# Kernel optimization log

Measured on AMD Instinct MI355X. Metric: run time of the kernel, lower is better.

The kernel has to match this reference:

```python
import jax, jax.numpy as jnp
import numpy as np

EPS = 1e-8
NUM_HEADS = 8
SCALE = 25.0
SIM_THRESH = 0.75
BLOCK = 10  # per-frame proposal group size used by the zeroing mask


def _l2norm(x):
    return x / (jnp.linalg.norm(x, axis=-1, keepdims=True) + EPS)


def setup_inputs() -> dict:
    key = jax.random.key(0)
    ks = jax.random.split(key, 7)
    B, N, C = 1, 2000, 256
    H = NUM_HEADS
    x_cls = jax.random.normal(ks[0], (B, N, C), dtype=jnp.float32)
    x_reg = jax.random.normal(ks[1], (B, N, C), dtype=jnp.float32)
    cls_score = jax.random.uniform(ks[2], (N,), dtype=jnp.float32)
    fg_score = jax.random.uniform(ks[3], (N,), dtype=jnp.float32)
    coord_attn = jax.random.uniform(ks[4], (B, H, N, N), dtype=jnp.float32)
    W_qkv_cls = jax.random.normal(ks[5], (3 * C, C), dtype=jnp.float32) * 0.02
    W_qkv_reg = jax.random.normal(ks[6], (3 * C, C), dtype=jnp.float32) * 0.02
    return {"x_cls": x_cls, "x_reg": x_reg, "cls_score": cls_score,
            "fg_score": fg_score, "coord_attn": coord_attn,
            "W_qkv_cls": W_qkv_cls, "W_qkv_reg": W_qkv_reg}


def reference(x_cls, x_reg, cls_score, fg_score, coord_attn, W_qkv_cls, W_qkv_reg):
    B, N, C = x_cls.shape
    H = NUM_HEADS
    D = C // H

    def qkv(x, W):
        t = (x @ W.T).reshape(B, N, 3, H, D).transpose(2, 0, 3, 1, 4)  # [3,B,H,N,D]
        return t[0], t[1], t[2]

    q_cls, k_cls, v_cls = qkv(x_cls, W_qkv_cls)
    q_reg, k_reg, v_reg = qkv(x_reg, W_qkv_reg)

    q_cls, k_cls = _l2norm(q_cls), _l2norm(k_cls)
    q_reg, k_reg = _l2norm(q_reg), _l2norm(k_reg)
    v_cls_normed = _l2norm(v_cls)

    cs = cls_score.reshape(1, 1, 1, N)  # broadcast over [B,H,N,N]
    fs = fg_score.reshape(1, 1, 1, N)

    attn_cls_raw = jnp.einsum('bhnd,bhmd->bhnm', v_cls_normed, v_cls_normed)

    attn_cls = jax.nn.softmax(jnp.einsum('bhnd,bhmd->bhnm', q_cls, k_cls) * SCALE * cs, axis=-1)
    attn_reg = jax.nn.softmax(jnp.einsum('bhnd,bhmd->bhnm', q_reg, k_reg) * SCALE * fs, axis=-1)

    attn = (attn_reg + attn_cls) * 0.5 * coord_attn
    attn = jax.lax.stop_gradient(attn)  # original detaches before masking

    # block-diagonal zeroing: row j zeros cols [j//10*10, j//10*10+9), keep diagonal
    rows = jnp.arange(N)[:, None]
    cols = jnp.arange(N)[None, :]
    block_start = (rows // BLOCK) * BLOCK
    zero_mask = (cols >= block_start) & (cols < block_start + (BLOCK - 1)) & (cols != rows)
    attn = jnp.where(zero_mask, 0.0, attn)

    x = jnp.einsum('bhnm,bhmd->bhnd', attn, v_cls).transpose(0, 2, 1, 3).reshape(B, N, C)
    x_ori = v_cls.transpose(0, 2, 1, 3).reshape(B, N, C)
    x_cat = jnp.concatenate([x, x_ori], axis=-1)  # [B,N,2C]

    # ave=True branch
    sim_raw = jnp.sum(attn_cls_raw, axis=1)[0] / H          # [N,N]
    sim_mask = (sim_raw > SIM_THRESH).astype(x_cls.dtype)
    sim_attn = jnp.sum(attn, axis=1)[0] / H                 # [N,N]
    sim_round2 = jax.nn.softmax(sim_attn, axis=-1)
    sim_round2 = sim_mask * sim_round2 / (jnp.sum(sim_mask * sim_round2, axis=-1, keepdims=True) + EPS)
    return x_cat, sim_round2
```

## Files before the change

kernel.cpp:

```cpp
#include <hip/hip_runtime.h>
#include <math.h>

typedef _Float16 half8 __attribute__((ext_vector_type(8)));
typedef _Float16 half4 __attribute__((ext_vector_type(4)));
typedef _Float16 half2v __attribute__((ext_vector_type(2)));
typedef float f32x4 __attribute__((ext_vector_type(4)));

constexpr int N = 2000;
constexpr int NP = 2048;
constexpr int H = 8;
constexpr int D = 32;
constexpr float SCL = 25.0f;
constexpr float L2E = 1.4426950408889634f;
constexpr float FM2 = 25.0f * L2E;

#define MFMA16(a,b,c)  __builtin_amdgcn_mfma_f32_16x16x32_f16((a),(b),(c),0,0,0)
#define MFMA16K(a,b,c) __builtin_amdgcn_mfma_f32_16x16x16f16((a),(b),(c),0,0,0)

__device__ __forceinline__ float fexp2(float x) { return __builtin_amdgcn_exp2f(x); }


__global__ __launch_bounds__(256) void wconv_kernel(
    const float* __restrict__ Wc, const float* __restrict__ Wr,
    _Float16* __restrict__ Wch, _Float16* __restrict__ Wrh)
{
    const int i = blockIdx.x * 256 + threadIdx.x;
    Wch[i] = (_Float16)Wc[i];
    Wrh[i] = (_Float16)Wr[i];
}

__global__ __launch_bounds__(256) void qkv_kernel(
    const float* __restrict__ xc, const float* __restrict__ xr,
    const _Float16* __restrict__ Wch, const _Float16* __restrict__ Wrh,
    const float* __restrict__ clsScore, const float* __restrict__ fgScore,
    _Float16* __restrict__ Qch, _Float16* __restrict__ Kch,
    _Float16* __restrict__ Qrh, _Float16* __restrict__ Krh,
    _Float16* __restrict__ Vnh, _Float16* __restrict__ Vth,
    float* __restrict__ out)
{
    constexpr int XS = 264;
    __shared__ _Float16 xs[16 * XS];
    const int t = threadIdx.x;
    const int n0 = blockIdx.x * 16;
    const int by = blockIdx.y;
    const int which = (by < 3) ? by : (by - 3);
    const bool isCls = by < 3;
    const float* x = isCls ? xc : xr;
    const _Float16* Wh = isCls ? Wch : Wrh;

    #pragma unroll
    for (int it = 0; it < 4; ++it) {
        const int f = t + it * 256;
        const int row = f >> 6, c4 = f & 63;
        const float4 v = *(const float4*)(x + (size_t)(n0 + row) * 256 + c4 * 4);
        half4 hv; hv[0]=(_Float16)v.x; hv[1]=(_Float16)v.y; hv[2]=(_Float16)v.z; hv[3]=(_Float16)v.w;
        *(half4*)&xs[row * XS + c4 * 4] = hv;
    }
    __syncthreads();

    const int w = t >> 6, l = t & 63;
    const int lr = l & 15, lg = l >> 4;
    const int obase = which * 256 + w * 64;
    f32x4 acc[4] = {{0,0,0,0},{0,0,0,0},{0,0,0,0},{0,0,0,0}};
    for (int k0 = 0; k0 < 256; k0 += 32) {
        const half8 aX = *(const half8*)&xs[lr * XS + k0 + lg * 8];
        #pragma unroll
        for (int s = 0; s < 4; ++s) {
            const half8 bW = *(const half8*)(Wh + (size_t)(obase + s * 16 + lr) * 256 + k0 + lg * 8);
            acc[s] = MFMA16(aX, bW, acc[s]);
        }
    }
    f32x4 kscale = {1.f,1.f,1.f,1.f};
    if (which == 1) {
        const float* sp = isCls ? clsScore : fgScore;
        kscale = (SCL * L2E) * *(const f32x4*)(sp + n0 + lg*4);
    }
    #pragma unroll
    for (int p = 0; p < 2; ++p) {
        const int h = 2 * w + p;
        float ss[4];
        #pragma unroll
        for (int j = 0; j < 4; ++j) {
            float v = acc[2*p][j]*acc[2*p][j] + acc[2*p+1][j]*acc[2*p+1][j];
            #pragma unroll
            for (int off = 1; off < 16; off <<= 1) v += __shfl_xor(v, off);
            ss[j] = sqrtf(v) + 1e-8f;
        }
        if (which < 2) {
            _Float16* Qd = isCls ? (which == 0 ? Qch : Kch) : (which == 0 ? Qrh : Krh);
            #pragma unroll
            for (int sh = 0; sh < 2; ++sh)
                #pragma unroll
                for (int j = 0; j < 4; ++j)
                    Qd[((size_t)h*NP + n0 + lg*4 + j)*D + sh*16 + lr]
                        = (_Float16)(acc[2*p+sh][j] / ss[j] * kscale[j]);
        } else {
            #pragma unroll
            for (int sh = 0; sh < 2; ++sh) {
                const int d = sh * 16 + lr;
                half4 tv;
                #pragma unroll
                for (int j = 0; j < 4; ++j) {
                    const float raw = acc[2*p+sh][j];
                    Vnh[((size_t)h*NP + n0 + lg*4 + j)*D + d] = (_Float16)(raw / ss[j]);
                    out[(size_t)(n0 + lg*4 + j)*512 + 256 + h*D + d] = raw;
                    tv[j] = (_Float16)raw;
                }
                *(half4*)(Vth + ((size_t)h*D + d)*NP + n0 + lg*4) = tv;
            }
        }
    }
}

__global__ __launch_bounds__(512) void stats_kernel(
    const _Float16* __restrict__ Qch, const _Float16* __restrict__ Kch,
    const _Float16* __restrict__ Qrh, const _Float16* __restrict__ Krh,
    float* __restrict__ BIAS)
{
    __shared__ float Ssh[2][4][16];
    const int t = threadIdx.x;
    const int w = t >> 6, l = t & 63;
    const int nsub = w >> 2, mq = w & 3;
    const int n0 = blockIdx.x * 32 + nsub * 16;
    const int h = blockIdx.y, z = blockIdx.z;
    const _Float16* Q = z ? Qrh : Qch;
    const _Float16* K = z ? Krh : Kch;
    const int lr = l & 15, lg = l >> 4;
    const half8 aQ = *(const half8*)(Q + ((size_t)h*NP + n0 + lr)*D + lg*8);
    float S[4] = {0.f, 0.f, 0.f, 0.f};
    const int mqB0 = (mq == 0) ? 0 : 31*mq;
    const int mqB1 = (mq == 3) ? 125 : 31*(mq+1);
    half8 bK = *(const half8*)(K + ((size_t)h*NP + mqB0*16 + lr)*D + lg*8);
    for (int ms = mqB0; ms < mqB1; ++ms) {
        const half8 cur = bK;
        if (ms + 1 < mqB1)
            bK = *(const half8*)(K + ((size_t)h*NP + (ms+1)*16 + lr)*D + lg*8);
        f32x4 z4 = {0.f, 0.f, 0.f, 0.f};
        const f32x4 c = MFMA16(aQ, cur, z4);
        #pragma unroll
        for (int j = 0; j < 4; ++j) S[j] += fexp2(c[j] - FM2);
    }
    #pragma unroll
    for (int j = 0; j < 4; ++j) {
        #pragma unroll
        for (int off = 1; off < 16; off <<= 1) S[j] += __shfl_xor(S[j], off);
    }
    if (lr == 0) {
        #pragma unroll
        for (int j = 0; j < 4; ++j) Ssh[nsub][mq][lg*4 + j] = S[j];
    }
    __syncthreads();
    if (t < 32) {
        const int ns = t >> 4, rl = t & 15;
        const int n = blockIdx.x * 32 + ns*16 + rl;
        BIAS[((size_t)z*H + h)*NP + n]
            = -__log2f(Ssh[ns][0][rl] + Ssh[ns][1][rl] + Ssh[ns][2][rl] + Ssh[ns][3][rl]) - FM2 - 1.0f;
    }
}

__global__ __launch_bounds__(256) void vvmask_kernel(
    const _Float16* __restrict__ Vnh, unsigned char* __restrict__ Mask)
{
    const int t = threadIdx.x;
    const int w = t >> 6, l = t & 63;
    const int n0 = blockIdx.y * 16;
    const int m00 = blockIdx.x * 256 + w * 64;
    const int lr = l & 15, lg = l >> 4;
    half8 aV[8];
    #pragma unroll
    for (int h = 0; h < 8; ++h)
        aV[h] = *(const half8*)(Vnh + ((size_t)(h*NP + n0 + lr))*D + lg*8);
    for (int s = 0; s < 4; ++s) {
        const int mb = m00 + s*16;
        f32x4 acc = {0.f, 0.f, 0.f, 0.f};
        #pragma unroll
        for (int h = 0; h < 8; ++h) {
            const half8 bV = *(const half8*)(Vnh + ((size_t)(h*NP + mb + lr))*D + lg*8);
            acc = MFMA16(aV[h], bV, acc);
        }
        const int m = mb + lr;
        if (m < N) {
            #pragma unroll
            for (int j = 0; j < 4; ++j) {
                const int n = n0 + lg*4 + j;
                Mask[(size_t)n*N + m] = (acc[j]*0.125f > 0.75f) ? (unsigned char)1 : (unsigned char)0;
            }
        }
    }
}

__global__ __launch_bounds__(256) void attn_kernel(
    const _Float16* __restrict__ Kch, const _Float16* __restrict__ Krh,
    const _Float16* __restrict__ Qch, const _Float16* __restrict__ Qrh,
    const _Float16* __restrict__ Vth, const float* __restrict__ coord,
    const float* __restrict__ BIAS,
    _Float16* __restrict__ SIMH, _Float16* __restrict__ XPH)
{
    __shared__ __align__(16) float costage[2][2048];
    __shared__ _Float16 pvred[2][4][2][16][18];

    const int t = threadIdx.x;
    const int w = t >> 6, l = t & 63;
    const int lr = l & 15, lg = l >> 4;
    const int mc = blockIdx.x;
    const int m0 = mc * 128;
    const int n0 = blockIdx.y * 16;
    const int n  = n0 + lr;
    const int bs = (n / 10) * 10;
    const int s0 = w * 2;

    unsigned kill = 0u;
    #pragma unroll
    for (int sl = 0; sl < 2; ++sl)
        #pragma unroll
        for (int j = 0; j < 4; ++j) {
            const int m = m0 + (s0 + sl)*16 + lg*4 + j;
            if ((m >= bs && m < bs + 9 && m != n) || m >= N) kill |= (1u << (sl*4 + j));
        }

    const int drow = w*4 + (l >> 4);
    const int dck  = l & 15;
    auto DMACO = [&](int hp) {
        float* dst = &costage[hp & 1][0];
        #pragma unroll
        for (int i = 0; i < 2; ++i) {
            const int colb = i*64 + ((((dck*16) ^ ((drow & 7) << 4))) >> 2);
            unsigned gi = (unsigned)((hp*N + (n0 + drow))*N + m0 + colb);
            gi = gi < 31999996u ? gi : 31999996u;
            __builtin_amdgcn_global_load_lds(
                (const __attribute__((address_space(1))) void*)(coord + gi),
                (__attribute__((address_space(3))) void*)(dst + i*1024 + w*256),
                16, 0, 0);
        }
    };

    half8 aQc[2], aQr[2]; float bC[2], bR[2];
    auto LOADQ = [&](int hp) {
        const int hb = hp & 1;
        aQc[hb] = *(const half8*)(Qch + ((size_t)hp*NP + n)*D + lg*8);
        aQr[hb] = *(const half8*)(Qrh + ((size_t)hp*NP + n)*D + lg*8);
        bC[hb]  = BIAS[(size_t)hp*NP + n];
        bR[hb]  = BIAS[(size_t)(H + hp)*NP + n];
    };

    half8 kc[2], kr[2]; half4 v0[2], v1[2];
    auto LOADKV = [&](int hp, int sl, int b) {
        const int m = m0 + (s0 + sl)*16;
        const size_t kb = ((size_t)hp*NP + m + lr)*D + lg*8;
        kc[b] = *(const half8*)(Kch + kb);
        kr[b] = *(const half8*)(Krh + kb);
        v0[b] = *(const half4*)(Vth + ((size_t)(hp*D + lr))*NP + m + lg*4);
        v1[b] = *(const half4*)(Vth + ((size_t)(hp*D + 16 + lr))*NP + m + lg*4);
    };

    float sacc[2][4] = {{0,0,0,0},{0,0,0,0}};

    DMACO(0); LOADQ(0);
    __builtin_amdgcn_sched_barrier(0);
    LOADKV(0, 0, 0);
    asm volatile("s_waitcnt vmcnt(4)" ::: "memory");
    __builtin_amdgcn_s_barrier();
    __builtin_amdgcn_sched_barrier(0);

    #pragma unroll
    for (int h = 0; h < H; ++h) {
        const int hb = h & 1;
        if (h + 1 < H) { DMACO(h + 1); LOADQ(h + 1); }
        __builtin_amdgcn_sched_barrier(0);
        f32x4 pv0 = {0,0,0,0}, pv1 = {0,0,0,0};
        #pragma unroll
        for (int sl = 0; sl < 2; ++sl) {
            const int b = (h*2 + sl) & 1;
            if (sl == 0)            LOADKV(h, 1, b ^ 1);
            else if (h + 1 < H)     LOADKV(h + 1, 0, b ^ 1);
            const int s = s0 + sl;
            const int cbyte = (((s & 3)*64 + lg*16) ^ ((lr & 7) << 4));
            const f32x4 co = *(const f32x4*)(&costage[hb][(s >> 2)*1024 + lr*64] + (cbyte >> 2));
            f32x4 z4 = {0,0,0,0};
            const f32x4 cc = MFMA16(kc[b], aQc[hb], z4);
            const f32x4 cr = MFMA16(kr[b], aQr[hb], z4);
            half4 af;
            #pragma unroll
            for (int j = 0; j < 4; ++j) {
                float a = (fexp2(cc[j] + bC[hb]) + fexp2(cr[j] + bR[hb])) * co[j];
                if ((kill >> (sl*4 + j)) & 1u) a = 0.f;
                sacc[sl][j] += a;
                af[j] = (_Float16)a;
            }
            pv0 = MFMA16K(af, v0[b], pv0);
            pv1 = MFMA16K(af, v1[b], pv1);
        }
        {
            half4 h0v, h1v;
            #pragma unroll
            for (int j = 0; j < 4; ++j) { h0v[j] = (_Float16)pv0[j]; h1v[j] = (_Float16)pv1[j]; }
            *(half4*)&pvred[hb][w][0][lr][lg*4] = h0v;
            *(half4*)&pvred[hb][w][1][lr][lg*4] = h1v;
        }
        asm volatile("s_waitcnt vmcnt(4) lgkmcnt(0)" ::: "memory");
        __builtin_amdgcn_s_barrier();
        __builtin_amdgcn_sched_barrier(0);
        {
            const int e0 = 2*t;
            const int d = e0 & 15, db = (e0 >> 4) & 1, q = e0 >> 5;
            const float u0 = (float)pvred[hb][0][db][d][q]   + (float)pvred[hb][1][db][d][q]
                           + (float)pvred[hb][2][db][d][q]   + (float)pvred[hb][3][db][d][q];
            const float u1 = (float)pvred[hb][0][db][d+1][q] + (float)pvred[hb][1][db][d+1][q]
                           + (float)pvred[hb][2][db][d+1][q] + (float)pvred[hb][3][db][d+1][q];
            half2v o; o[0] = (_Float16)u0; o[1] = (_Float16)u1;
            *(half2v*)(XPH + ((size_t)(mc*H + h)*N + n0)*D + e0) = o;
        }
    }

    #pragma unroll
    for (int sl = 0; sl < 2; ++sl) {
        const int mbase = m0 + (s0 + sl)*16;
        if (mbase < N) {
            half4 sv;
            #pragma unroll
            for (int j = 0; j < 4; ++j) sv[j] = (_Float16)sacc[sl][j];
            *(half4*)(SIMH + (size_t)n*N + mbase + lg*4) = sv;
        }
    }
}

__global__ __launch_bounds__(256) void reduce_kernel(
    const _Float16* __restrict__ XPH, float* __restrict__ out)
{
    const int n = blockIdx.x, t = threadIdx.x;
    const int h = t >> 5, d = t & 31;
    float acc = 0.f;
    #pragma unroll
    for (int mcI = 0; mcI < 16; ++mcI)
        acc += (float)XPH[(((size_t)mcI*H + h)*N + n)*D + d];
    out[(size_t)n*512 + t] = acc;
}

__global__ __launch_bounds__(256) void simfinal_kernel(
    const _Float16* __restrict__ SIMH, const unsigned char* __restrict__ Mask,
    float* __restrict__ out)
{
    __shared__ float redA[4], redB[4];
    const int n = blockIdx.x, t = threadIdx.x;
    const _Float16* row = SIMH + (size_t)n * N;
    const unsigned char* mrow = Mask + (size_t)n * N;
    const bool act = t < 250;
    float f[8];
    unsigned int mk0 = 0, mk1 = 0;
    float mx = -1e30f;
    if (act) {
        const half8 v8 = *(const half8*)(row + t*8);
        const uint2 mm = *(const uint2*)(mrow + t*8);
        mk0 = mm.x; mk1 = mm.y;
        #pragma unroll
        for (int k = 0; k < 8; ++k) { f[k] = (float)v8[k]; mx = fmaxf(mx, f[k]); }
    }
    #pragma unroll
    for (int off = 1; off < 64; off <<= 1) mx = fmaxf(mx, __shfl_xor(mx, off));
    const int wv = t >> 6;
    if ((t & 63) == 0) redA[wv] = mx;
    __syncthreads();
    const float M = fmaxf(fmaxf(redA[0], redA[1]), fmaxf(redA[2], redA[3]));
    float e[8];
    float sA = 0.f, sM = 0.f;
    if (act) {
        #pragma unroll
        for (int k = 0; k < 8; ++k) {
            e[k] = fexp2((f[k] - M) * (L2E * 0.125f));
            sA += e[k];
            const unsigned int mkb = ((k < 4 ? mk0 : mk1) >> (8*(k & 3))) & 0xffu;
            if (mkb) sM += e[k]; else e[k] = 0.f;
        }
    }
    #pragma unroll
    for (int off = 1; off < 64; off <<= 1) { sA += __shfl_xor(sA, off); sM += __shfl_xor(sM, off); }
    __syncthreads();
    if ((t & 63) == 0) { redA[wv] = sA; redB[wv] = sM; }
    __syncthreads();
    const float SA = redA[0] + redA[1] + redA[2] + redA[3];
    const float SMK = redB[0] + redB[1] + redB[2] + redB[3];
    const float inv = 1.f / (SMK + 1e-8f * SA);
    if (act) {
        float* orow = out + 1024000 + (size_t)n*N + t*8;
        *(float4*)(orow)     = make_float4(e[0]*inv, e[1]*inv, e[2]*inv, e[3]*inv);
        *(float4*)(orow + 4) = make_float4(e[4]*inv, e[5]*inv, e[6]*inv, e[7]*inv);
    }
}

extern "C" void kernel_launch(void* const* d_in, const int* in_sizes, int n_in,
                              void* d_out, int out_size, void* d_ws, size_t ws_size,
                              hipStream_t stream) {
    const float* x_cls     = (const float*)d_in[0];
    const float* x_reg     = (const float*)d_in[1];
    const float* cls_score = (const float*)d_in[2];
    const float* fg_score  = (const float*)d_in[3];
    const float* coord     = (const float*)d_in[4];
    const float* Wc        = (const float*)d_in[5];
    const float* Wr        = (const float*)d_in[6];

    char* base = (char*)d_ws;
    float* BIAS     = (float*)base;
    _Float16* SIMH  = (_Float16*)(base + 131072);
    _Float16* XPH   = (_Float16*)(base + 8131072);
    _Float16* Qch   = (_Float16*)(base + 24515072);
    _Float16* Kch   = Qch + 524288;
    _Float16* Qrh   = Qch + 2*524288;
    _Float16* Krh   = Qch + 3*524288;
    _Float16* Vnh   = Qch + 4*524288;
    _Float16* Vth   = Qch + 5*524288;
    _Float16* Wch   = (_Float16*)(base + 30806528);
    _Float16* Wrh   = (_Float16*)(base + 31199744);
    unsigned char* Mask = (unsigned char*)(base + 31592960);
    float* out = (float*)d_out;

    wconv_kernel<<<768, 256, 0, stream>>>(Wc, Wr, Wch, Wrh);
    qkv_kernel<<<dim3(125, 5), 256, 0, stream>>>(x_cls, x_reg, Wch, Wrh, cls_score, fg_score,
                                                 Qch, Kch, Qrh, Krh, Vnh, Vth, out);
    stats_kernel<<<dim3(63, 8, 2), 512, 0, stream>>>(Qch, Kch, Qrh, Krh, BIAS);
    vvmask_kernel<<<dim3(8, 125), 256, 0, stream>>>(Vnh, Mask);
    attn_kernel<<<dim3(16, 125), 256, 0, stream>>>(Kch, Krh, Qch, Qrh, Vth, coord,
                                                   BIAS, SIMH, XPH);
    reduce_kernel<<<2000, 256, 0, stream>>>(XPH, out);
    simfinal_kernel<<<2000, 256, 0, stream>>>(SIMH, Mask, out);
}
```

Before: 134.6 us.

## Split fused attention into probability materialization and separate PV kernels per head half

The fused attention kernel, which staged coord through LDS with async DMA and reduced PV partials across m-chunks through a workspace, is split up. A pattn kernel now writes fp16 probabilities for four heads at a time to a 32 MB buffer. A pv kernel then does the full PV reduction per row directly into the output, which removes the XPH partial buffer and the reduce kernel. The aim is simpler kernels with higher occupancy and no cross-chunk reduction, at the cost of writing and re-reading a large probability matrix and giving up the software prefetch pipeline.

```diff
diff --git a/kernel.cpp b/kernel.cpp
--- a/kernel.cpp
+++ b/kernel.cpp
@@ -3,7 +3,6 @@
 
 typedef _Float16 half8 __attribute__((ext_vector_type(8)));
 typedef _Float16 half4 __attribute__((ext_vector_type(4)));
-typedef _Float16 half2v __attribute__((ext_vector_type(2)));
 typedef float f32x4 __attribute__((ext_vector_type(4)));
 
 constexpr int N = 2000;
@@ -189,171 +188,153 @@
     }
 }
 
-__global__ __launch_bounds__(256) void attn_kernel(
+__global__ __launch_bounds__(256, 6) void pattn_kernel(
     const _Float16* __restrict__ Kch, const _Float16* __restrict__ Krh,
     const _Float16* __restrict__ Qch, const _Float16* __restrict__ Qrh,
-    const _Float16* __restrict__ Vth, const float* __restrict__ coord,
-    const float* __restrict__ BIAS,
-    _Float16* __restrict__ SIMH, _Float16* __restrict__ XPH)
-{
-    __shared__ __align__(16) float costage[2][2048];
-    __shared__ _Float16 pvred[2][4][2][16][18];
-
+    const float* __restrict__ coord, const float* __restrict__ BIAS,
+    _Float16* __restrict__ Pout, _Float16* __restrict__ SIMH, int hbase)
+{
     const int t = threadIdx.x;
     const int w = t >> 6, l = t & 63;
     const int lr = l & 15, lg = l >> 4;
-    const int mc = blockIdx.x;
-    const int m0 = mc * 128;
+    const int m0 = blockIdx.x * 128;
     const int n0 = blockIdx.y * 16;
     const int n  = n0 + lr;
     const int bs = (n / 10) * 10;
-    const int s0 = w * 2;
-
+    const int s0 = 2 * w;
+
+    int mb[2]; bool ok[2];
     unsigned kill = 0u;
     #pragma unroll
-    for (int sl = 0; sl < 2; ++sl)
+    for (int sl = 0; sl < 2; ++sl) {
+        mb[sl] = m0 + (s0 + sl)*16;
+        ok[sl] = mb[sl] < N;
         #pragma unroll
         for (int j = 0; j < 4; ++j) {
-            const int m = m0 + (s0 + sl)*16 + lg*4 + j;
-            if ((m >= bs && m < bs + 9 && m != n) || m >= N) kill |= (1u << (sl*4 + j));
-        }
-
-    const int drow = w*4 + (l >> 4);
-    const int dck  = l & 15;
-    auto DMACO = [&](int hp) {
-        float* dst = &costage[hp & 1][0];
-        #pragma unroll
-        for (int i = 0; i < 2; ++i) {
-            const int colb = i*64 + ((((dck*16) ^ ((drow & 7) << 4))) >> 2);
-            unsigned gi = (unsigned)((hp*N + (n0 + drow))*N + m0 + colb);
-            gi = gi < 31999996u ? gi : 31999996u;
-            __builtin_amdgcn_global_load_lds(
-                (const __attribute__((address_space(1))) void*)(coord + gi),
-                (__attribute__((address_space(3))) void*)(dst + i*1024 + w*256),
-                16, 0, 0);
-        }
-    };
-
-    half8 aQc[2], aQr[2]; float bC[2], bR[2];
-    auto LOADQ = [&](int hp) {
-        const int hb = hp & 1;
-        aQc[hb] = *(const half8*)(Qch + ((size_t)hp*NP + n)*D + lg*8);
-        aQr[hb] = *(const half8*)(Qrh + ((size_t)hp*NP + n)*D + lg*8);
-        bC[hb]  = BIAS[(size_t)hp*NP + n];
-        bR[hb]  = BIAS[(size_t)(H + hp)*NP + n];
-    };
-
-    half8 kc[2], kr[2]; half4 v0[2], v1[2];
-    auto LOADKV = [&](int hp, int sl, int b) {
-        const int m = m0 + (s0 + sl)*16;
-        const size_t kb = ((size_t)hp*NP + m + lr)*D + lg*8;
-        kc[b] = *(const half8*)(Kch + kb);
-        kr[b] = *(const half8*)(Krh + kb);
-        v0[b] = *(const half4*)(Vth + ((size_t)(hp*D + lr))*NP + m + lg*4);
-        v1[b] = *(const half4*)(Vth + ((size_t)(hp*D + 16 + lr))*NP + m + lg*4);
-    };
+            const int m = mb[sl] + lg*4 + j;
+            if (m >= bs && m < bs + 9 && m != n) kill |= (1u << (sl*4 + j));
+        }
+    }
 
     float sacc[2][4] = {{0,0,0,0},{0,0,0,0}};
 
-    DMACO(0); LOADQ(0);
-    __builtin_amdgcn_sched_barrier(0);
-    LOADKV(0, 0, 0);
-    asm volatile("s_waitcnt vmcnt(4)" ::: "memory");
-    __builtin_amdgcn_s_barrier();
-    __builtin_amdgcn_sched_barrier(0);
-
-    #pragma unroll
-    for (int h = 0; h < H; ++h) {
-        const int hb = h & 1;
-        if (h + 1 < H) { DMACO(h + 1); LOADQ(h + 1); }
-        __builtin_amdgcn_sched_barrier(0);
-        f32x4 pv0 = {0,0,0,0}, pv1 = {0,0,0,0};
+    #pragma unroll
+    for (int hp = 0; hp < 4; ++hp) {
+        const int h = hbase + hp;
+        const float bC = BIAS[(size_t)h*NP + n];
+        const float bR = BIAS[(size_t)(H + h)*NP + n];
+        const half8 aQc = *(const half8*)(Qch + ((size_t)h*NP + n)*D + lg*8);
+        const half8 aQr = *(const half8*)(Qrh + ((size_t)h*NP + n)*D + lg*8);
         #pragma unroll
         for (int sl = 0; sl < 2; ++sl) {
-            const int b = (h*2 + sl) & 1;
-            if (sl == 0)            LOADKV(h, 1, b ^ 1);
-            else if (h + 1 < H)     LOADKV(h + 1, 0, b ^ 1);
-            const int s = s0 + sl;
-            const int cbyte = (((s & 3)*64 + lg*16) ^ ((lr & 7) << 4));
-            const f32x4 co = *(const f32x4*)(&costage[hb][(s >> 2)*1024 + lr*64] + (cbyte >> 2));
+            const int m = mb[sl];
+            const half8 kc = *(const half8*)(Kch + ((size_t)h*NP + m + lr)*D + lg*8);
+            const half8 kr = *(const half8*)(Krh + ((size_t)h*NP + m + lr)*D + lg*8);
+            size_t gi = ((size_t)h*N + n)*N + m + lg*4;
+            if (!ok[sl]) gi = 0;
+            const f32x4 co = *(const f32x4*)(coord + gi);
             f32x4 z4 = {0,0,0,0};
-            const f32x4 cc = MFMA16(kc[b], aQc[hb], z4);
-            const f32x4 cr = MFMA16(kr[b], aQr[hb], z4);
+            const f32x4 cc = MFMA16(kc, aQc, z4);
+            const f32x4 cr = MFMA16(kr, aQr, z4);
             half4 af;
             #pragma unroll
             for (int j = 0; j < 4; ++j) {
-                float a = (fexp2(cc[j] + bC[hb]) + fexp2(cr[j] + bR[hb])) * co[j];
+                float a = (fexp2(cc[j] + bC) + fexp2(cr[j] + bR)) * co[j];
                 if ((kill >> (sl*4 + j)) & 1u) a = 0.f;
                 sacc[sl][j] += a;
                 af[j] = (_Float16)a;
             }
-            pv0 = MFMA16K(af, v0[b], pv0);
-            pv1 = MFMA16K(af, v1[b], pv1);
-        }
+            if (ok[sl])
+                *(half4*)(Pout + ((size_t)hp*N + n)*N + m + lg*4) = af;
+        }
+    }
+
+    #pragma unroll
+    for (int sl = 0; sl < 2; ++sl) {
+        if (!ok[sl]) continue;
+        half4 sv;
+        #pragma unroll
+        for (int j = 0; j < 4; ++j) sv[j] = (_Float16)sacc[sl][j];
+        *(half4*)(SIMH + (size_t)n*N + mb[sl] + lg*4) = sv;
+    }
+}
+
+__global__ __launch_bounds__(256) void pv_kernel(
+    const _Float16* __restrict__ P, const _Float16* __restrict__ Vth,
+    float* __restrict__ out, int hbase)
+{
+    __shared__ _Float16 pvred[4][2][16][18];
+    const int t = threadIdx.x;
+    const int w = t >> 6, l = t & 63;
+    const int lr = l & 15, lg = l >> 4;
+    const int n0 = blockIdx.x * 16;
+    const int hl = blockIdx.y;
+    const int h  = hbase + hl;
+    const int n  = n0 + lr;
+
+    const _Float16* prow = P + ((size_t)hl*N + n)*N;
+    const _Float16* v0row = Vth + ((size_t)(h*D + lr))*NP;
+    const _Float16* v1row = Vth + ((size_t)(h*D + 16 + lr))*NP;
+
+    f32x4 aA0 = {0,0,0,0}, aA1 = {0,0,0,0}, aB0 = {0,0,0,0}, aB1 = {0,0,0,0};
+    for (int ms = w; ms < 125; ms += 8) {
         {
-            half4 h0v, h1v;
-            #pragma unroll
-            for (int j = 0; j < 4; ++j) { h0v[j] = (_Float16)pv0[j]; h1v[j] = (_Float16)pv1[j]; }
-            *(half4*)&pvred[hb][w][0][lr][lg*4] = h0v;
-            *(half4*)&pvred[hb][w][1][lr][lg*4] = h1v;
-        }
-        asm volatile("s_waitcnt vmcnt(4) lgkmcnt(0)" ::: "memory");
-        __builtin_amdgcn_s_barrier();
-        __builtin_amdgcn_sched_barrier(0);
-        {
-            const int e0 = 2*t;
-            const int d = e0 & 15, db = (e0 >> 4) & 1, q = e0 >> 5;
-            const float u0 = (float)pvred[hb][0][db][d][q]   + (float)pvred[hb][1][db][d][q]
-                           + (float)pvred[hb][2][db][d][q]   + (float)pvred[hb][3][db][d][q];
-            const float u1 = (float)pvred[hb][0][db][d+1][q] + (float)pvred[hb][1][db][d+1][q]
-                           + (float)pvred[hb][2][db][d+1][q] + (float)pvred[hb][3][db][d+1][q];
-            half2v o; o[0] = (_Float16)u0; o[1] = (_Float16)u1;
-            *(half2v*)(XPH + ((size_t)(mc*H + h)*N + n0)*D + e0) = o;
-        }
-    }
-
-    #pragma unroll
-    for (int sl = 0; sl < 2; ++sl) {
-        const int mbase = m0 + (s0 + sl)*16;
-        if (mbase < N) {
-            half4 sv;
-            #pragma unroll
-            for (int j = 0; j < 4; ++j) sv[j] = (_Float16)sacc[sl][j];
-            *(half4*)(SIMH + (size_t)n*N + mbase + lg*4) = sv;
-        }
-    }
-}
-
-__global__ __launch_bounds__(256) void reduce_kernel(
-    const _Float16* __restrict__ XPH, float* __restrict__ out)
-{
-    const int n = blockIdx.x, t = threadIdx.x;
-    const int h = t >> 5, d = t & 31;
-    float acc = 0.f;
-    #pragma unroll
-    for (int mcI = 0; mcI < 16; ++mcI)
-        acc += (float)XPH[(((size_t)mcI*H + h)*N + n)*D + d];
-    out[(size_t)n*512 + t] = acc;
+            const int m = ms*16;
+            const half4 af = *(const half4*)(prow + m + lg*4);
+            const half4 v0 = *(const half4*)(v0row + m + lg*4);
+            const half4 v1 = *(const half4*)(v1row + m + lg*4);
+            aA0 = MFMA16K(af, v0, aA0);
+            aA1 = MFMA16K(af, v1, aA1);
+        }
+        const int ms2 = ms + 4;
+        if (ms2 < 125) {
+            const int m = ms2*16;
+            const half4 af = *(const half4*)(prow + m + lg*4);
+            const half4 v0 = *(const half4*)(v0row + m + lg*4);
+            const half4 v1 = *(const half4*)(v1row + m + lg*4);
+            aB0 = MFMA16K(af, v0, aB0);
+            aB1 = MFMA16K(af, v1, aB1);
+        }
+    }
+    const f32x4 pv0 = aA0 + aB0;
+    const f32x4 pv1 = aA1 + aB1;
+    {
+        half4 h0v, h1v;
+        #pragma unroll
+        for (int j = 0; j < 4; ++j) { h0v[j] = (_Float16)pv0[j]; h1v[j] = (_Float16)pv1[j]; }
+        *(half4*)&pvred[w][0][lr][lg*4] = h0v;
+        *(half4*)&pvred[w][1][lr][lg*4] = h1v;
+    }
+    __syncthreads();
+    {
+        const int e0 = 2*t;
+        const int d = e0 & 15, db = (e0 >> 4) & 1, q = e0 >> 5;
+        const float u0 = (float)pvred[0][db][d][q]   + (float)pvred[1][db][d][q]
+                       + (float)pvred[2][db][d][q]   + (float)pvred[3][db][d][q];
+        const float u1 = (float)pvred[0][db][d+1][q] + (float)pvred[1][db][d+1][q]
+                       + (float)pvred[2][db][d+1][q] + (float)pvred[3][db][d+1][q];
+        *(float2*)(out + (size_t)(n0 + q)*512 + h*32 + db*16 + d) = make_float2(u0, u1);
+    }
 }
 
 __global__ __launch_bounds__(256) void simfinal_kernel(
-    const _Float16* __restrict__ SIMH, const unsigned char* __restrict__ Mask,
-    float* __restrict__ out)
+    const _Float16* __restrict__ SIMH0, const _Float16* __restrict__ SIMH1,
+    const unsigned char* __restrict__ Mask, float* __restrict__ out)
 {
     __shared__ float redA[4], redB[4];
     const int n = blockIdx.x, t = threadIdx.x;
-    const _Float16* row = SIMH + (size_t)n * N;
     const unsigned char* mrow = Mask + (size_t)n * N;
     const bool act = t < 250;
     float f[8];
     unsigned int mk0 = 0, mk1 = 0;
     float mx = -1e30f;
     if (act) {
-        const half8 v8 = *(const half8*)(row + t*8);
+        const half8 va = *(const half8*)(SIMH0 + (size_t)n*N + t*8);
+        const half8 vb = *(const half8*)(SIMH1 + (size_t)n*N + t*8);
         const uint2 mm = *(const uint2*)(mrow + t*8);
         mk0 = mm.x; mk1 = mm.y;
         #pragma unroll
-        for (int k = 0; k < 8; ++k) { f[k] = (float)v8[k]; mx = fmaxf(mx, f[k]); }
+        for (int k = 0; k < 8; ++k) { f[k] = (float)va[k] + (float)vb[k]; mx = fmaxf(mx, f[k]); }
     }
     #pragma unroll
     for (int off = 1; off < 64; off <<= 1) mx = fmaxf(mx, __shfl_xor(mx, off));
@@ -399,18 +380,19 @@
     const float* Wr        = (const float*)d_in[6];
 
     char* base = (char*)d_ws;
-    float* BIAS     = (float*)base;
-    _Float16* SIMH  = (_Float16*)(base + 131072);
-    _Float16* XPH   = (_Float16*)(base + 8131072);
-    _Float16* Qch   = (_Float16*)(base + 24515072);
-    _Float16* Kch   = Qch + 524288;
-    _Float16* Qrh   = Qch + 2*524288;
-    _Float16* Krh   = Qch + 3*524288;
-    _Float16* Vnh   = Qch + 4*524288;
-    _Float16* Vth   = Qch + 5*524288;
-    _Float16* Wch   = (_Float16*)(base + 30806528);
-    _Float16* Wrh   = (_Float16*)(base + 31199744);
-    unsigned char* Mask = (unsigned char*)(base + 31592960);
+    float* BIAS      = (float*)base;
+    _Float16* SIMH0  = (_Float16*)(base + 131072);
+    _Float16* SIMH1  = (_Float16*)(base + 8131072);
+    _Float16* P      = (_Float16*)(base + 16131072);
+    _Float16* Qch    = (_Float16*)(base + 48131072);
+    _Float16* Kch    = Qch + 524288;
+    _Float16* Qrh    = Qch + 2*524288;
+    _Float16* Krh    = Qch + 3*524288;
+    _Float16* Vnh    = Qch + 4*524288;
+    _Float16* Vth    = Qch + 5*524288;
+    _Float16* Wch    = (_Float16*)(base + 54422528);
+    _Float16* Wrh    = (_Float16*)(base + 54815744);
+    unsigned char* Mask = (unsigned char*)(base + 55208960);
     float* out = (float*)d_out;
 
     wconv_kernel<<<768, 256, 0, stream>>>(Wc, Wr, Wch, Wrh);
@@ -418,8 +400,11 @@
                                                  Qch, Kch, Qrh, Krh, Vnh, Vth, out);
     stats_kernel<<<dim3(63, 8, 2), 512, 0, stream>>>(Qch, Kch, Qrh, Krh, BIAS);
     vvmask_kernel<<<dim3(8, 125), 256, 0, stream>>>(Vnh, Mask);
-    attn_kernel<<<dim3(16, 125), 256, 0, stream>>>(Kch, Krh, Qch, Qrh, Vth, coord,
-                                                   BIAS, SIMH, XPH);
-    reduce_kernel<<<2000, 256, 0, stream>>>(XPH, out);
-    simfinal_kernel<<<2000, 256, 0, stream>>>(SIMH, Mask, out);
-}
+
+    pattn_kernel<<<dim3(16, 125), 256, 0, stream>>>(Kch, Krh, Qch, Qrh, coord, BIAS, P, SIMH0, 0);
+    pv_kernel<<<dim3(125, 4), 256, 0, stream>>>(P, Vth, out, 0);
+    pattn_kernel<<<dim3(16, 125), 256, 0, stream>>>(Kch, Krh, Qch, Qrh, coord, BIAS, P, SIMH1, 4);
+    pv_kernel<<<dim3(125, 4), 256, 0, stream>>>(P, Vth, out, 4);
+
+    simfinal_kernel<<<2000, 256, 0, stream>>>(SIMH0, SIMH1, Mask, out);
+}
```

Result: slower. 159.6 us (+18.6%).
